# Kernel tuning notes

Measured on AMD Instinct MI355X. Metric: run time of the kernel, lower is better.

Reference implementation:

```python
import jax, jax.numpy as jnp
import numpy as np

N, E, F, H, L = 50000, 800000, 128, 128, 3
BN_EPS = 1e-5


def setup_inputs() -> dict:
    key = jax.random.key(0)
    ks = jax.random.split(key, 10)
    x = jax.random.normal(ks[0], (N, F), dtype=jnp.float32)
    edge_index = jax.random.randint(ks[1], (2, E), 0, N, dtype=jnp.int32)
    batch = jnp.sort(jax.random.randint(ks[2], (N,), 0, 64, dtype=jnp.int32))
    s1 = 1.0 / np.sqrt(F)
    s2 = 1.0 / np.sqrt(H)
    W1 = jax.random.uniform(ks[3], (L, F, H), jnp.float32, -s1, s1)
    b1 = jax.random.uniform(ks[4], (L, H), jnp.float32, -s1, s1)
    W2 = jax.random.uniform(ks[5], (L, H, H), jnp.float32, -s2, s2)
    b2 = jax.random.uniform(ks[6], (L, H), jnp.float32, -s2, s2)
    gamma = jnp.ones((L, H), jnp.float32)
    beta = jnp.zeros((L, H), jnp.float32)
    return {"x": x, "edge_index": edge_index, "batch": batch,
            "W1": W1, "b1": b1, "W2": W2, "b2": b2,
            "gamma": gamma, "beta": beta}


def _gin_layer(h, src, dst, n_nodes, W1, b1, W2, b2, g, be):
    # GINConv, eps=0: h_i <- MLP(h_i + sum_{j->i} h_j)
    agg = jax.ops.segment_sum(h[src], dst, num_segments=n_nodes)
    h2 = h + agg
    h2 = jax.nn.relu(h2 @ W1 + b1)
    h2 = jax.nn.relu(h2 @ W2 + b2)
    # BatchNorm1d (training-mode batch stats, biased variance)
    mu = jnp.mean(h2, axis=0)
    var = jnp.mean(jnp.square(h2 - mu), axis=0)
    return g * (h2 - mu) * jax.lax.rsqrt(var + BN_EPS) + be


def reference(x, edge_index, batch, W1, b1, W2, b2, gamma, beta):
    src, dst = edge_index[0], edge_index[1]
    n_nodes = x.shape[0]
    h = x
    for l in range(W1.shape[0]):  # small fixed layer count
        h = _gin_layer(h, src, dst, n_nodes, W1[l], b1[l], W2[l], b2[l], gamma[l], beta[l])
    # JumpingKnowledge(mode='last') returns final layer output
    return (h, batch)
```

## Files before the change

### kernel.cpp

```cpp
#include <hip/hip_runtime.h>
#include <hip/hip_bf16.h>

constexpr int NF = 128;
constexpr int BM = 128;
constexpr int SORT_CHUNK = 4096;
constexpr float BN_EPS_C = 1e-5f;

typedef __attribute__((ext_vector_type(8))) short short8;
typedef __attribute__((ext_vector_type(4))) float f32x4;

__device__ __forceinline__ float asfloat(unsigned int u) {
  union { unsigned int u; float f; } c; c.u = u; return c.f;
}
__device__ __forceinline__ unsigned short f2b(float f) {
  __hip_bfloat16 b = __float2bfloat16(f);
  return *reinterpret_cast<unsigned short*>(&b);
}
__device__ __forceinline__ void addbf8(float* acc, uint4 v) {
  acc[0] += asfloat(v.x << 16); acc[1] += asfloat(v.x & 0xffff0000u);
  acc[2] += asfloat(v.y << 16); acc[3] += asfloat(v.y & 0xffff0000u);
  acc[4] += asfloat(v.z << 16); acc[5] += asfloat(v.z & 0xffff0000u);
  acc[6] += asfloat(v.w << 16); acc[7] += asfloat(v.w & 0xffff0000u);
}

__global__ __launch_bounds__(256)
void p1_hist(const int* __restrict__ dst, int* __restrict__ ghist,
             int E, int B1, int nbins1)
{
  __shared__ int hist[256];
  int tid = threadIdx.x, blk = blockIdx.x;
  hist[tid] = 0;
  __syncthreads();
  int base = blk * SORT_CHUNK;
  int end_ = min(E, base + SORT_CHUNK);
  for (int i = base + tid; i < end_; i += 256)
    atomicAdd(&hist[dst[i] >> 8], 1);
  __syncthreads();
  if (tid < nbins1) ghist[tid * B1 + blk] = hist[tid];
}

__global__ __launch_bounds__(256)
void scan1(const int* __restrict__ count, int* __restrict__ excl,
           int* __restrict__ bsum, int n)
{
  __shared__ int s[256];
  int tid = threadIdx.x;
  int i = blockIdx.x * 256 + tid;
  int v = (i < n) ? count[i] : 0;
  s[tid] = v;
  __syncthreads();
  #pragma unroll
  for (int d = 1; d < 256; d <<= 1) {
    int t = (tid >= d) ? s[tid - d] : 0;
    __syncthreads();
    s[tid] += t;
    __syncthreads();
  }
  if (i < n) excl[i] = s[tid] - v;
  if (tid == 255) bsum[blockIdx.x] = s[255];
}

__global__ __launch_bounds__(256)
void scan2(int* __restrict__ bsum, int nb)
{
  __shared__ int s[256];
  int tid = threadIdx.x;
  int v = (tid < nb) ? bsum[tid] : 0;
  s[tid] = v;
  __syncthreads();
  #pragma unroll
  for (int d = 1; d < 256; d <<= 1) {
    int t = (tid >= d) ? s[tid - d] : 0;
    __syncthreads();
    s[tid] += t;
    __syncthreads();
  }
  if (tid < nb) bsum[tid] = s[tid] - v;
}

__global__ __launch_bounds__(256)
void scan_add(int* __restrict__ data, const int* __restrict__ bsum, int n)
{
  int i = blockIdx.x * 256 + threadIdx.x;
  if (i < n) data[i] += bsum[blockIdx.x];
}

__global__ __launch_bounds__(256)
void p1_scatter(const int* __restrict__ src, const int* __restrict__ dst,
                const int* __restrict__ goff, int2* __restrict__ tmp,
                int E, int B1, int nbins1)
{
  __shared__ int cur[256];
  int tid = threadIdx.x, blk = blockIdx.x;
  if (tid < nbins1) cur[tid] = goff[tid * B1 + blk];
  __syncthreads();
  int base = blk * SORT_CHUNK;
  int end_ = min(E, base + SORT_CHUNK);
  for (int i = base + tid; i < end_; i += 256) {
    int d = dst[i];
    int pos = atomicAdd(&cur[d >> 8], 1);
    tmp[pos] = make_int2(src[i], d);
  }
}

__global__ __launch_bounds__(256)
void p2_sort(const int2* __restrict__ tmp, const int* __restrict__ goff,
             int* __restrict__ adj, int* __restrict__ row_off,
             int E, int B1, int nbins1, int N)
{
  __shared__ int hist[256], s[256], cur[256];
  int H = blockIdx.x, tid = threadIdx.x;
  int base = goff[H * B1];
  int end_ = (H + 1 < nbins1) ? goff[(H + 1) * B1] : E;

  hist[tid] = 0;
  __syncthreads();
  for (int i = base + tid; i < end_; i += 256)
    atomicAdd(&hist[tmp[i].y & 255], 1);
  __syncthreads();
  int v = hist[tid];
  s[tid] = v;
  __syncthreads();
  #pragma unroll
  for (int d = 1; d < 256; d <<= 1) {
    int t = (tid >= d) ? s[tid - d] : 0;
    __syncthreads();
    s[tid] += t;
    __syncthreads();
  }
  int excl = s[tid] - v;
  cur[tid] = base + excl;
  int node = H * 256 + tid;
  if (node < N)  row_off[node] = base + excl;
  if (node == N) row_off[N] = E;
  if (H == 0 && tid == 0 && (N & 255) == 0) row_off[N] = E;
  __syncthreads();
  for (int i = base + tid; i < end_; i += 256) {
    int2 p = tmp[i];
    int pos = atomicAdd(&cur[p.y & 255], 1);
    adj[pos] = p.x;
  }
}

__global__ __launch_bounds__(256)
void w_to_bf16t(const float* __restrict__ W, unsigned short* __restrict__ out, int total)
{
  int idx = blockIdx.x * 256 + threadIdx.x;
  if (idx >= total) return;
  int m = idx >> 14, ck = idx & 16383, c = ck >> 7, k = ck & 127;
  out[idx] = f2b(W[m * 16384 + k * 128 + c]);
}

__global__ __launch_bounds__(256)
void x_to_bf16(const float* __restrict__ x, unsigned short* __restrict__ xb, long long n4)
{
  long long i = (long long)blockIdx.x * 256 + threadIdx.x;
  if (i >= n4) return;
  float4 v = ((const float4*)x)[i];
  ushort4 o;
  o.x = f2b(v.x); o.y = f2b(v.y); o.z = f2b(v.z); o.w = f2b(v.w);
  ((ushort4*)xb)[i] = o;
}

__global__ void init_ss(float* __restrict__ ss)
{
  ss[threadIdx.x] = (threadIdx.x < NF) ? 1.f : 0.f;
}

__global__ __launch_bounds__(256)
void gather_bn(const unsigned short* __restrict__ h, const int* __restrict__ row_off,
               const int* __restrict__ adj, const float* __restrict__ ss,
               unsigned short* __restrict__ agg, int n)
{
  int wv  = threadIdx.x >> 6;
  int l   = threadIdx.x & 63;
  int sub = l >> 4, llo = l & 15;
  int node = blockIdx.x * 4 + wv;
  if (node >= n) return;
  int beg = row_off[node], end = row_off[node + 1];

  float acc[8] = {0.f, 0.f, 0.f, 0.f, 0.f, 0.f, 0.f, 0.f};
  if (sub == 0)
    addbf8(acc, *(const uint4*)(h + (size_t)node * NF + llo * 8));

  int e = beg + sub;
  for (; e + 12 < end; e += 16) {
    int s0 = adj[e], s1 = adj[e + 4], s2 = adj[e + 8], s3 = adj[e + 12];
    uint4 v0 = *(const uint4*)(h + (size_t)s0 * NF + llo * 8);
    uint4 v1 = *(const uint4*)(h + (size_t)s1 * NF + llo * 8);
    uint4 v2 = *(const uint4*)(h + (size_t)s2 * NF + llo * 8);
    uint4 v3 = *(const uint4*)(h + (size_t)s3 * NF + llo * 8);
    addbf8(acc, v0); addbf8(acc, v1); addbf8(acc, v2); addbf8(acc, v3);
  }
  for (; e < end; e += 4)
    addbf8(acc, *(const uint4*)(h + (size_t)adj[e] * NF + llo * 8));

  #pragma unroll
  for (int j = 0; j < 8; ++j) {
    acc[j] += __shfl_xor(acc[j], 16, 64);
    acc[j] += __shfl_xor(acc[j], 32, 64);
  }

  if (sub == 0) {
    float dp1 = (float)(end - beg + 1);
    unsigned short r[8];
    #pragma unroll
    for (int j = 0; j < 8; ++j) {
      float sc = ss[llo * 8 + j];
      float sh = ss[NF + llo * 8 + j];
      r[j] = f2b(fmaf(acc[j], sc, dp1 * sh));
    }
    uint4 o;
    o.x = (unsigned)r[0] | ((unsigned)r[1] << 16);
    o.y = (unsigned)r[2] | ((unsigned)r[3] << 16);
    o.z = (unsigned)r[4] | ((unsigned)r[5] << 16);
    o.w = (unsigned)r[6] | ((unsigned)r[7] << 16);
    *(uint4*)(agg + (size_t)node * NF + llo * 8) = o;
  }
}

template<bool LAST>
__global__ __launch_bounds__(256)
void gemm12(const unsigned short* __restrict__ agg,
            const unsigned short* __restrict__ w1t, const float* __restrict__ b1,
            const unsigned short* __restrict__ w2t, const float* __restrict__ b2,
            float* __restrict__ vout, unsigned short* __restrict__ vb16,
            double* __restrict__ part, int nrows, int nblk)
{
  __shared__ __align__(16) unsigned short Alds[BM * NF];

  const int tid = threadIdx.x;
  const int wid = tid >> 6;
  const int l   = tid & 63;
  const int lhi = l >> 4;
  const int llo = l & 15;
  const int row0 = blockIdx.x * BM;

  #pragma unroll
  for (int i = 0; i < 8; ++i) {
    int fidx = tid + 256 * i;
    int r = fidx >> 4, c16 = fidx & 15;
    int grow = row0 + r;
    uint4 v = make_uint4(0u, 0u, 0u, 0u);
    if (grow < nrows) v = *(const uint4*)(agg + (size_t)grow * NF + c16 * 8);
    int off = r * 256 + ((c16 * 16) ^ ((r & 7) << 4));
    *(uint4*)((char*)Alds + off) = v;
  }

  float b1v[8], b2v[8];
  #pragma unroll
  for (int c = 0; c < 8; ++c) {
    b1v[c] = b1[c * 16 + llo];
    b2v[c] = b2[c * 16 + llo];
  }

  const short8* w1v = (const short8*)w1t;
  const short8* w2v = (const short8*)w2t;

  f32x4 acc[2][8];
  #pragma unroll
  for (int s = 0; s < 2; ++s)
    #pragma unroll
    for (int c = 0; c < 8; ++c) acc[s][c] = (f32x4){0.f, 0.f, 0.f, 0.f};

  __syncthreads();

  #pragma unroll
  for (int t = 0; t < 4; ++t) {
    short8 af[2];
    #pragma unroll
    for (int s = 0; s < 2; ++s) {
      int r = wid * 32 + s * 16 + llo;
      int off = r * 256 + ((t * 64 + lhi * 16) ^ ((r & 7) << 4));
      af[s] = *(const short8*)((const char*)Alds + off);
    }
    #pragma unroll
    for (int c = 0; c < 8; ++c) {
      short8 bf = w1v[(c * 16 + llo) * 16 + t * 4 + lhi];
      acc[0][c] = __builtin_amdgcn_mfma_f32_16x16x32_bf16(af[0], bf, acc[0][c], 0, 0, 0);
      acc[1][c] = __builtin_amdgcn_mfma_f32_16x16x32_bf16(af[1], bf, acc[1][c], 0, 0, 0);
    }
  }

  __syncthreads();

  #pragma unroll
  for (int s = 0; s < 2; ++s)
    #pragma unroll
    for (int c = 0; c < 8; ++c) {
      int colg = c * 16 + llo;
      #pragma unroll
      for (int q = 0; q < 4; ++q) {
        int r = wid * 32 + s * 16 + lhi * 4 + q;
        float u = fmaxf(acc[s][c][q] + b1v[c], 0.f);
        int off = r * 256 + ((colg * 2) ^ ((r & 7) << 4));
        *(unsigned short*)((char*)Alds + off) = f2b(u);
      }
    }
  #pragma unroll
  for (int s = 0; s < 2; ++s)
    #pragma unroll
    for (int c = 0; c < 8; ++c) acc[s][c] = (f32x4){0.f, 0.f, 0.f, 0.f};

  __syncthreads();

  #pragma unroll
  for (int t = 0; t < 4; ++t) {
    short8 af[2];
    #pragma unroll
    for (int s = 0; s < 2; ++s) {
      int r = wid * 32 + s * 16 + llo;
      int off = r * 256 + ((t * 64 + lhi * 16) ^ ((r & 7) << 4));
      af[s] = *(const short8*)((const char*)Alds + off);
    }
    #pragma unroll
    for (int c = 0; c < 8; ++c) {
      short8 bf = w2v[(c * 16 + llo) * 16 + t * 4 + lhi];
      acc[0][c] = __builtin_amdgcn_mfma_f32_16x16x32_bf16(af[0], bf, acc[0][c], 0, 0, 0);
      acc[1][c] = __builtin_amdgcn_mfma_f32_16x16x32_bf16(af[1], bf, acc[1][c], 0, 0, 0);
    }
  }

  float ts[8] = {0.f, 0.f, 0.f, 0.f, 0.f, 0.f, 0.f, 0.f};
  float tq[8] = {0.f, 0.f, 0.f, 0.f, 0.f, 0.f, 0.f, 0.f};
  #pragma unroll
  for (int s = 0; s < 2; ++s)
    #pragma unroll
    for (int c = 0; c < 8; ++c) {
      int colg = c * 16 + llo;
      #pragma unroll
      for (int q = 0; q < 4; ++q) {
        int rloc = wid * 32 + s * 16 + lhi * 4 + q;
        int row = row0 + rloc;
        if (row < nrows) {
          float vv = fmaxf(acc[s][c][q] + b2v[c], 0.f);
          ts[c] += vv; tq[c] += vv * vv;
          if (LAST) vout[(size_t)row * NF + colg] = vv;
          else      vb16[(size_t)row * NF + colg] = f2b(vv);
        }
      }
    }

  __syncthreads();
  double* redS = (double*)Alds;
  double* redQ = redS + 16 * NF;
  int prow = wid * 4 + lhi;
  #pragma unroll
  for (int c = 0; c < 8; ++c) {
    redS[prow * NF + c * 16 + llo] = (double)ts[c];
    redQ[prow * NF + c * 16 + llo] = (double)tq[c];
  }
  __syncthreads();
  if (tid < NF) {
    double s = 0.0;
    #pragma unroll
    for (int r = 0; r < 16; ++r) s += redS[r * NF + tid];
    part[(size_t)blockIdx.x * NF + tid] = s;
  } else {
    int c = tid - NF;
    double s = 0.0;
    #pragma unroll
    for (int r = 0; r < 16; ++r) s += redQ[r * NF + c];
    part[(size_t)nblk * NF + (size_t)blockIdx.x * NF + c] = s;
  }
}

__global__ __launch_bounds__(1024)
void bn_stats_final(const double* __restrict__ part,
                    const float* __restrict__ gamma,
                    const float* __restrict__ beta,
                    float* __restrict__ ss, int nrows, int nblk)
{
  __shared__ double redS[64][17], redQ[64][17];
  int cl  = threadIdx.x & 15;
  int seg = threadIdx.x >> 4;
  int c = blockIdx.x * 16 + cl;
  double s = 0.0, s2 = 0.0;
  for (int b = seg; b < nblk; b += 64) {
    s  += part[(size_t)b * NF + c];
    s2 += part[(size_t)nblk * NF + (size_t)b * NF + c];
  }
  redS[seg][cl] = s;
  redQ[seg][cl] = s2;
  __syncthreads();
  #pragma unroll
  for (int d = 32; d >= 1; d >>= 1) {
    if (seg < d) {
      redS[seg][cl] += redS[seg + d][cl];
      redQ[seg][cl] += redQ[seg + d][cl];
    }
    __syncthreads();
  }
  if (seg == 0) {
    double invN = 1.0 / (double)nrows;
    double mu  = redS[0][cl] * invN;
    double var = redQ[0][cl] * invN - mu * mu;
    double sc  = (double)gamma[c] / sqrt(var + (double)BN_EPS_C);
    ss[c]      = (float)sc;
    ss[NF + c] = (float)((double)beta[c] - mu * sc);
  }
}

__global__ __launch_bounds__(256)
void bn_apply(const float* __restrict__ v, const float* __restrict__ ss,
              float* __restrict__ out, int nrows)
{
  long long i = (long long)blockIdx.x * 256 + threadIdx.x;
  long long total = (long long)nrows * (NF / 4);
  if (i >= total) return;
  int c = (int)(i & 31) * 4;
  float4 val = ((const float4*)v)[i];
  float4 o;
  o.x = fmaf(val.x, ss[c + 0], ss[NF + c + 0]);
  o.y = fmaf(val.y, ss[c + 1], ss[NF + c + 1]);
  o.z = fmaf(val.z, ss[c + 2], ss[NF + c + 2]);
  o.w = fmaf(val.w, ss[c + 3], ss[NF + c + 3]);
  ((float4*)out)[i] = o;
}

__global__ void copy_batch(const int* __restrict__ b, float* __restrict__ o, int n)
{
  int i = blockIdx.x * 256 + threadIdx.x;
  if (i < n) o[i] = (float)b[i];
}

extern "C" void kernel_launch(void* const* d_in, const int* in_sizes, int n_in,
                              void* d_out, int out_size, void* d_ws, size_t ws_size,
                              hipStream_t stream)
{
  const float* x     = (const float*)d_in[0];
  const int*   ei    = (const int*)  d_in[1];
  const int*   batch = (const int*)  d_in[2];
  const float* W1    = (const float*)d_in[3];
  const float* b1    = (const float*)d_in[4];
  const float* W2    = (const float*)d_in[5];
  const float* b2    = (const float*)d_in[6];
  const float* gamma = (const float*)d_in[7];
  const float* beta  = (const float*)d_in[8];

  const int N = in_sizes[2];
  const int E = in_sizes[1] / 2;
  const int L = in_sizes[4] / NF;

  const int* src = ei;
  const int* dst = ei + E;

  const int nblk   = (N + BM - 1) / BM;
  const int B1     = (E + SORT_CHUNK - 1) / SORT_CHUNK;
  const int nbins1 = (N + 255) >> 8;
  const int nscan  = nbins1 * B1;
  const int scanBlocks = (nscan + 255) / 256;

  double* part = (double*)d_ws;
  float*  ss   = (float*)(part + 2 * (size_t)nblk * NF);
  unsigned short* aggb = (unsigned short*)(ss + 256);
  unsigned short* vb   = aggb + (size_t)N * NF;
  unsigned short* wt   = vb + (size_t)N * NF;
  int* row_off = (int*)(wt + 6 * 16384);
  int* adj     = row_off + (N + 1);
  int2* tmp   = (int2*)aggb;
  int*  ghist = (int*)vb;
  int*  goff  = ghist + nscan;
  int*  bsum  = goff + nscan;

  float* vbuf = (float*)d_out;
  float* outBatch = vbuf + (size_t)N * NF;
  unsigned short* xb = (unsigned short*)vbuf;

  const int nBlocks256 = (N + 255) / 256;
  const int bnBlocks   = (int)(((long long)N * (NF / 4) + 255) / 256);
  const long long x4   = (long long)N * NF / 4;

  x_to_bf16<<<(int)((x4 + 255) / 256), 256, 0, stream>>>(x, xb, x4);
  init_ss<<<1, 256, 0, stream>>>(ss);
  w_to_bf16t<<<(3 * 16384 + 255) / 256, 256, 0, stream>>>(W1, wt, 3 * 16384);
  w_to_bf16t<<<(3 * 16384 + 255) / 256, 256, 0, stream>>>(W2, wt + 3 * 16384, 3 * 16384);

  p1_hist<<<B1, 256, 0, stream>>>(dst, ghist, E, B1, nbins1);
  scan1<<<scanBlocks, 256, 0, stream>>>(ghist, goff, bsum, nscan);
  scan2<<<1, 256, 0, stream>>>(bsum, scanBlocks);
  scan_add<<<scanBlocks, 256, 0, stream>>>(goff, bsum, nscan);
  p1_scatter<<<B1, 256, 0, stream>>>(src, dst, goff, tmp, E, B1, nbins1);
  p2_sort<<<nbins1, 256, 0, stream>>>(tmp, goff, adj, row_off, E, B1, nbins1, N);

  for (int ly = 0; ly < L; ++ly) {
    const unsigned short* hsrc = (ly == 0) ? xb : vb;
    gather_bn<<<(N + 3) / 4, 256, 0, stream>>>(hsrc, row_off, adj, ss, aggb, N);

    const unsigned short* w1t = wt + (size_t)ly * 16384;
    const unsigned short* w2t = wt + (size_t)(3 + ly) * 16384;
    if (ly == L - 1)
      gemm12<true><<<nblk, 256, 0, stream>>>(aggb, w1t, b1 + ly * NF, w2t, b2 + ly * NF,
                                             vbuf, vb, part, N, nblk);
    else
      gemm12<false><<<nblk, 256, 0, stream>>>(aggb, w1t, b1 + ly * NF, w2t, b2 + ly * NF,
                                              vbuf, vb, part, N, nblk);
    bn_stats_final<<<8, 1024, 0, stream>>>(part, gamma + ly * NF, beta + ly * NF,
                                           ss, N, nblk);
  }

  bn_apply<<<bnBlocks, 256, 0, stream>>>(vbuf, ss, vbuf, N);
  copy_batch<<<nBlocks256, 256, 0, stream>>>(batch, outBatch, N);
}
```

Measured before the change: 249.1 us.

## Halve GEMM row tile, pack sort pairs, merge small launches

Shrinks the fused two-layer MLP GEMM tile from 128 to 64 rows per block, so each wave owns one 16-row MFMA strip. This halves LDS and accumulator registers, raising occupancy and doubling block count, but each block reloads the weights for half as many rows. The edge sort now packs the source and low destination byte into one 32-bit word instead of an int2, halving temp traffic. The two weight-conversion launches are merged into one, and the BN-apply and batch-copy kernels are merged into one.

```diff
diff --git a/kernel.cpp b/kernel.cpp
--- a/kernel.cpp
+++ b/kernel.cpp
@@ -2,7 +2,7 @@
 #include <hip/hip_bf16.h>
 
 constexpr int NF = 128;
-constexpr int BM = 128;
+constexpr int BM = 64;
 constexpr int SORT_CHUNK = 4096;
 constexpr float BN_EPS_C = 1e-5f;
 
@@ -87,7 +87,7 @@
 
 __global__ __launch_bounds__(256)
 void p1_scatter(const int* __restrict__ src, const int* __restrict__ dst,
-                const int* __restrict__ goff, int2* __restrict__ tmp,
+                const int* __restrict__ goff, unsigned* __restrict__ tmp,
                 int E, int B1, int nbins1)
 {
   __shared__ int cur[256];
@@ -99,12 +99,12 @@
   for (int i = base + tid; i < end_; i += 256) {
     int d = dst[i];
     int pos = atomicAdd(&cur[d >> 8], 1);
-    tmp[pos] = make_int2(src[i], d);
-  }
-}
-
-__global__ __launch_bounds__(256)
-void p2_sort(const int2* __restrict__ tmp, const int* __restrict__ goff,
+    tmp[pos] = ((unsigned)src[i] << 8) | (unsigned)(d & 255);
+  }
+}
+
+__global__ __launch_bounds__(256)
+void p2_sort(const unsigned* __restrict__ tmp, const int* __restrict__ goff,
              int* __restrict__ adj, int* __restrict__ row_off,
              int E, int B1, int nbins1, int N)
 {
@@ -116,7 +116,7 @@
   hist[tid] = 0;
   __syncthreads();
   for (int i = base + tid; i < end_; i += 256)
-    atomicAdd(&hist[tmp[i].y & 255], 1);
+    atomicAdd(&hist[(int)(tmp[i] & 255u)], 1);
   __syncthreads();
   int v = hist[tid];
   s[tid] = v;
@@ -136,18 +136,21 @@
   if (H == 0 && tid == 0 && (N & 255) == 0) row_off[N] = E;
   __syncthreads();
   for (int i = base + tid; i < end_; i += 256) {
-    int2 p = tmp[i];
-    int pos = atomicAdd(&cur[p.y & 255], 1);
-    adj[pos] = p.x;
-  }
-}
-
-__global__ __launch_bounds__(256)
-void w_to_bf16t(const float* __restrict__ W, unsigned short* __restrict__ out, int total)
+    unsigned p = tmp[i];
+    int pos = atomicAdd(&cur[(int)(p & 255u)], 1);
+    adj[pos] = (int)(p >> 8);
+  }
+}
+
+__global__ __launch_bounds__(256)
+void w_to_bf16t2(const float* __restrict__ W1, const float* __restrict__ W2,
+                 unsigned short* __restrict__ out, int half)
 {
   int idx = blockIdx.x * 256 + threadIdx.x;
-  if (idx >= total) return;
-  int m = idx >> 14, ck = idx & 16383, c = ck >> 7, k = ck & 127;
+  if (idx >= 2 * half) return;
+  const float* W = (idx < half) ? W1 : W2;
+  int j = (idx < half) ? idx : idx - half;
+  int m = j >> 14, ck = j & 16383, c = ck >> 7, k = ck & 127;
   out[idx] = f2b(W[m * 16384 + k * 128 + c]);
 }
 
@@ -237,7 +240,7 @@
   const int row0 = blockIdx.x * BM;
 
   #pragma unroll
-  for (int i = 0; i < 8; ++i) {
+  for (int i = 0; i < 4; ++i) {
     int fidx = tid + 256 * i;
     int r = fidx >> 4, c16 = fidx & 15;
     int grow = row0 + r;
@@ -257,110 +260,97 @@
   const short8* w1v = (const short8*)w1t;
   const short8* w2v = (const short8*)w2t;
 
-  f32x4 acc[2][8];
-  #pragma unroll
-  for (int s = 0; s < 2; ++s)
-    #pragma unroll
-    for (int c = 0; c < 8; ++c) acc[s][c] = (f32x4){0.f, 0.f, 0.f, 0.f};
+  f32x4 acc[8];
+  #pragma unroll
+  for (int c = 0; c < 8; ++c) acc[c] = (f32x4){0.f, 0.f, 0.f, 0.f};
 
   __syncthreads();
 
   #pragma unroll
   for (int t = 0; t < 4; ++t) {
-    short8 af[2];
-    #pragma unroll
-    for (int s = 0; s < 2; ++s) {
-      int r = wid * 32 + s * 16 + llo;
-      int off = r * 256 + ((t * 64 + lhi * 16) ^ ((r & 7) << 4));
-      af[s] = *(const short8*)((const char*)Alds + off);
-    }
+    int r = wid * 16 + llo;
+    int off = r * 256 + ((t * 64 + lhi * 16) ^ ((r & 7) << 4));
+    short8 af = *(const short8*)((const char*)Alds + off);
     #pragma unroll
     for (int c = 0; c < 8; ++c) {
       short8 bf = w1v[(c * 16 + llo) * 16 + t * 4 + lhi];
-      acc[0][c] = __builtin_amdgcn_mfma_f32_16x16x32_bf16(af[0], bf, acc[0][c], 0, 0, 0);
-      acc[1][c] = __builtin_amdgcn_mfma_f32_16x16x32_bf16(af[1], bf, acc[1][c], 0, 0, 0);
-    }
-  }
-
-  __syncthreads();
-
-  #pragma unroll
-  for (int s = 0; s < 2; ++s)
-    #pragma unroll
-    for (int c = 0; c < 8; ++c) {
-      int colg = c * 16 + llo;
-      #pragma unroll
-      for (int q = 0; q < 4; ++q) {
-        int r = wid * 32 + s * 16 + lhi * 4 + q;
-        float u = fmaxf(acc[s][c][q] + b1v[c], 0.f);
-        int off = r * 256 + ((colg * 2) ^ ((r & 7) << 4));
-        *(unsigned short*)((char*)Alds + off) = f2b(u);
-      }
-    }
-  #pragma unroll
-  for (int s = 0; s < 2; ++s)
-    #pragma unroll
-    for (int c = 0; c < 8; ++c) acc[s][c] = (f32x4){0.f, 0.f, 0.f, 0.f};
+      acc[c] = __builtin_amdgcn_mfma_f32_16x16x32_bf16(af, bf, acc[c], 0, 0, 0);
+    }
+  }
+
+  __syncthreads();
+
+  #pragma unroll
+  for (int c = 0; c < 8; ++c) {
+    int colg = c * 16 + llo;
+    #pragma unroll
+    for (int q = 0; q < 4; ++q) {
+      int r = wid * 16 + lhi * 4 + q;
+      float u = fmaxf(acc[c][q] + b1v[c], 0.f);
+      int off = r * 256 + ((colg * 2) ^ ((r & 7) << 4));
+      *(unsigned short*)((char*)Alds + off) = f2b(u);
+    }
+  }
+  #pragma unroll
+  for (int c = 0; c < 8; ++c) acc[c] = (f32x4){0.f, 0.f, 0.f, 0.f};
 
   __syncthreads();
 
   #pragma unroll
   for (int t = 0; t < 4; ++t) {
-    short8 af[2];
-    #pragma unroll
-    for (int s = 0; s < 2; ++s) {
-      int r = wid * 32 + s * 16 + llo;
-      int off = r * 256 + ((t * 64 + lhi * 16) ^ ((r & 7) << 4));
-      af[s] = *(const short8*)((const char*)Alds + off);
-    }
+    int r = wid * 16 + llo;
+    int off = r * 256 + ((t * 64 + lhi * 16) ^ ((r & 7) << 4));
+    short8 af = *(const short8*)((const char*)Alds + off);
     #pragma unroll
     for (int c = 0; c < 8; ++c) {
       short8 bf = w2v[(c * 16 + llo) * 16 + t * 4 + lhi];
-      acc[0][c] = __builtin_amdgcn_mfma_f32_16x16x32_bf16(af[0], bf, acc[0][c], 0, 0, 0);
-      acc[1][c] = __builtin_amdgcn_mfma_f32_16x16x32_bf16(af[1], bf, acc[1][c], 0, 0, 0);
+      acc[c] = __builtin_amdgcn_mfma_f32_16x16x32_bf16(af, bf, acc[c], 0, 0, 0);
     }
   }
 
   float ts[8] = {0.f, 0.f, 0.f, 0.f, 0.f, 0.f, 0.f, 0.f};
   float tq[8] = {0.f, 0.f, 0.f, 0.f, 0.f, 0.f, 0.f, 0.f};
   #pragma unroll
-  for (int s = 0; s < 2; ++s)
+  for (int c = 0; c < 8; ++c) {
+    int colg = c * 16 + llo;
+    #pragma unroll
+    for (int q = 0; q < 4; ++q) {
+      int rloc = wid * 16 + lhi * 4 + q;
+      int row = row0 + rloc;
+      if (row < nrows) {
+        float vv = fmaxf(acc[c][q] + b2v[c], 0.f);
+        ts[c] += vv; tq[c] += vv * vv;
+        if (LAST) vout[(size_t)row * NF + colg] = vv;
+        else      vb16[(size_t)row * NF + colg] = f2b(vv);
+      }
+    }
+  }
+
+  #pragma unroll
+  for (int c = 0; c < 8; ++c) {
+    ts[c] += __shfl_xor(ts[c], 16, 64);
+    ts[c] += __shfl_xor(ts[c], 32, 64);
+    tq[c] += __shfl_xor(tq[c], 16, 64);
+    tq[c] += __shfl_xor(tq[c], 32, 64);
+  }
+
+  __syncthreads();
+  double* redS = (double*)Alds;
+  double* redQ = redS + 4 * NF;
+  if (lhi == 0) {
     #pragma unroll
     for (int c = 0; c < 8; ++c) {
-      int colg = c * 16 + llo;
-      #pragma unroll
-      for (int q = 0; q < 4; ++q) {
-        int rloc = wid * 32 + s * 16 + lhi * 4 + q;
-        int row = row0 + rloc;
-        if (row < nrows) {
-          float vv = fmaxf(acc[s][c][q] + b2v[c], 0.f);
-          ts[c] += vv; tq[c] += vv * vv;
-          if (LAST) vout[(size_t)row * NF + colg] = vv;
-          else      vb16[(size_t)row * NF + colg] = f2b(vv);
-        }
-      }
-    }
-
-  __syncthreads();
-  double* redS = (double*)Alds;
-  double* redQ = redS + 16 * NF;
-  int prow = wid * 4 + lhi;
-  #pragma unroll
-  for (int c = 0; c < 8; ++c) {
-    redS[prow * NF + c * 16 + llo] = (double)ts[c];
-    redQ[prow * NF + c * 16 + llo] = (double)tq[c];
+      redS[wid * NF + c * 16 + llo] = (double)ts[c];
+      redQ[wid * NF + c * 16 + llo] = (double)tq[c];
+    }
   }
   __syncthreads();
   if (tid < NF) {
-    double s = 0.0;
-    #pragma unroll
-    for (int r = 0; r < 16; ++r) s += redS[r * NF + tid];
+    double s = redS[tid] + redS[NF + tid] + redS[2 * NF + tid] + redS[3 * NF + tid];
     part[(size_t)blockIdx.x * NF + tid] = s;
   } else {
     int c = tid - NF;
-    double s = 0.0;
-    #pragma unroll
-    for (int r = 0; r < 16; ++r) s += redQ[r * NF + c];
+    double s = redQ[c] + redQ[NF + c] + redQ[2 * NF + c] + redQ[3 * NF + c];
     part[(size_t)nblk * NF + (size_t)blockIdx.x * NF + c] = s;
   }
 }
@@ -402,26 +392,25 @@
 }
 
 __global__ __launch_bounds__(256)
-void bn_apply(const float* __restrict__ v, const float* __restrict__ ss,
-              float* __restrict__ out, int nrows)
+void bn_apply_batch(const float* __restrict__ v, const float* __restrict__ ss,
+                    float* __restrict__ out, const int* __restrict__ batch,
+                    float* __restrict__ outBatch, int nrows)
 {
   long long i = (long long)blockIdx.x * 256 + threadIdx.x;
   long long total = (long long)nrows * (NF / 4);
-  if (i >= total) return;
-  int c = (int)(i & 31) * 4;
-  float4 val = ((const float4*)v)[i];
-  float4 o;
-  o.x = fmaf(val.x, ss[c + 0], ss[NF + c + 0]);
-  o.y = fmaf(val.y, ss[c + 1], ss[NF + c + 1]);
-  o.z = fmaf(val.z, ss[c + 2], ss[NF + c + 2]);
-  o.w = fmaf(val.w, ss[c + 3], ss[NF + c + 3]);
-  ((float4*)out)[i] = o;
-}
-
-__global__ void copy_batch(const int* __restrict__ b, float* __restrict__ o, int n)
-{
-  int i = blockIdx.x * 256 + threadIdx.x;
-  if (i < n) o[i] = (float)b[i];
+  if (i < total) {
+    int c = (int)(i & 31) * 4;
+    float4 val = ((const float4*)v)[i];
+    float4 o;
+    o.x = fmaf(val.x, ss[c + 0], ss[NF + c + 0]);
+    o.y = fmaf(val.y, ss[c + 1], ss[NF + c + 1]);
+    o.z = fmaf(val.z, ss[c + 2], ss[NF + c + 2]);
+    o.w = fmaf(val.w, ss[c + 3], ss[NF + c + 3]);
+    ((float4*)out)[i] = o;
+  } else {
+    long long j = i - total;
+    if (j < nrows) outBatch[j] = (float)batch[j];
+  }
 }
 
 extern "C" void kernel_launch(void* const* d_in, const int* in_sizes, int n_in,
@@ -458,7 +447,7 @@
   unsigned short* wt   = vb + (size_t)N * NF;
   int* row_off = (int*)(wt + 6 * 16384);
   int* adj     = row_off + (N + 1);
-  int2* tmp   = (int2*)aggb;
+  unsigned* tmp = (unsigned*)aggb;
   int*  ghist = (int*)vb;
   int*  goff  = ghist + nscan;
   int*  bsum  = goff + nscan;
@@ -467,14 +456,12 @@
   float* outBatch = vbuf + (size_t)N * NF;
   unsigned short* xb = (unsigned short*)vbuf;
 
-  const int nBlocks256 = (N + 255) / 256;
-  const int bnBlocks   = (int)(((long long)N * (NF / 4) + 255) / 256);
-  const long long x4   = (long long)N * NF / 4;
+  const long long x4 = (long long)N * NF / 4;
+  const long long bnTot = (long long)N * (NF / 4) + N;
 
   x_to_bf16<<<(int)((x4 + 255) / 256), 256, 0, stream>>>(x, xb, x4);
   init_ss<<<1, 256, 0, stream>>>(ss);
-  w_to_bf16t<<<(3 * 16384 + 255) / 256, 256, 0, stream>>>(W1, wt, 3 * 16384);
-  w_to_bf16t<<<(3 * 16384 + 255) / 256, 256, 0, stream>>>(W2, wt + 3 * 16384, 3 * 16384);
+  w_to_bf16t2<<<(6 * 16384 + 255) / 256, 256, 0, stream>>>(W1, W2, wt, 3 * 16384);
 
   p1_hist<<<B1, 256, 0, stream>>>(dst, ghist, E, B1, nbins1);
   scan1<<<scanBlocks, 256, 0, stream>>>(ghist, goff, bsum, nscan);
@@ -499,6 +486,6 @@
                                            ss, N, nblk);
   }
 
-  bn_apply<<<bnBlocks, 256, 0, stream>>>(vbuf, ss, vbuf, N);
-  copy_batch<<<nBlocks256, 256, 0, stream>>>(batch, outBatch, N);
-}
+  bn_apply_batch<<<(int)((bnTot + 255) / 256), 256, 0, stream>>>(
+      vbuf, ss, vbuf, batch, outBatch, N);
+}
```

Result: slower. 287.4 us (+15.4%).
